# Kernel optimization log

Measured on AMD Instinct MI355X. Metric: run time of the kernel, lower is better.

## Reference

```python
import jax, jax.numpy as jnp
import numpy as np

N = 100000   # nodes
E = 1600000  # edges (avg degree 16)
Q = 64       # mesoscale velocity bins
H = 64       # collision MLP hidden dim
DT = 0.1
REG = 1e-6


def setup_inputs() -> dict:
    key = jax.random.key(0)
    ks = jax.random.split(key, 10)
    return {
        "f": jax.random.uniform(ks[0], (N, Q), jnp.float32),
        "macro_u": jax.random.normal(ks[1], (N, 1), jnp.float32),
        "source": 0.01 * jax.random.normal(ks[2], (N, Q), jnp.float32),
        "edge_src": jax.random.randint(ks[3], (E,), 0, N, jnp.int32),
        "edge_dst": jax.random.randint(ks[4], (E,), 0, N, jnp.int32),
        "edge_w": jax.random.uniform(ks[5], (E,), jnp.float32),
        "xi": jnp.linspace(-1.0, 1.0, Q).astype(jnp.float32),
        "w_in": jax.random.normal(ks[6], (Q, H), jnp.float32) / np.float32(np.sqrt(Q)),
        "b_in": jnp.zeros((H,), jnp.float32),
        "w_hid": jax.random.normal(ks[7], (3, H, H), jnp.float32) / np.float32(np.sqrt(H)),
        "b_hid": jnp.zeros((3, H), jnp.float32),
        "w_out": jax.random.normal(ks[8], (H, Q), jnp.float32) / np.float32(np.sqrt(H)),
        "b_out": jnp.zeros((Q,), jnp.float32),
    }


def _collision(f, macro_u, xi, w_in, b_in, w_hid, b_hid, w_out, b_out):
    # 5-layer MLP: relu hidden, tanh output (CollisionOperator.forward)
    x = jax.nn.relu(f @ w_in + b_in)
    for i in range(3):  # fixed small layer count, not a data-dim loop
        x = jax.nn.relu(x @ w_hid[i] + b_hid[i])
    omega = jnp.tanh(x @ w_out + b_out)                     # [N, Q]
    # Hard collision-invariance constraint: Omega* = (I - C^T (C C^T)^-1 C) Omega
    q = f.shape[1]
    w = jnp.full((q,), 1.0 / q, f.dtype)                    # quadrature weights
    xi_shifted = xi[None, :] + macro_u                      # [N, Q]
    C = jnp.stack([jnp.broadcast_to(w, xi_shifted.shape), w * xi_shifted], axis=1)  # [N,2,Q]
    CCT = jnp.einsum('naq,nbq->nab', C, C) + REG * jnp.eye(2, dtype=f.dtype)        # [N,2,2]
    v = jnp.einsum('naq,nq->na', C, omega)                  # [N,2]
    s = jnp.linalg.solve(CCT, v[..., None])[..., 0]         # [N,2]  (== CCT^-1 v)
    return omega - jnp.einsum('naq,na->nq', C, s)           # avoid dense [N,Q,Q] projection


def _transport(f, xi, edge_src, edge_dst, edge_w, n):
    # BoltzmannUpdater.compute_transport_term: both inflow (on graph) and
    # outflow (on reverse graph) reduce to the same per-edge message
    #   m_e = (w_e / out_deg[src_e]) * xi * (f[dst_e] - f[src_e])
    # aggregated at dst (inflow) and at src (outflow); transport = outflow - inflow.
    out_deg = jax.ops.segment_sum(jnp.ones_like(edge_w), edge_src, num_segments=n)
    q_e = edge_w / out_deg[edge_src]                         # [E]
    msg = q_e[:, None] * xi[None, :] * (f[edge_dst] - f[edge_src])  # [E, Q]
    inflow = jax.ops.segment_sum(msg, edge_dst, num_segments=n)
    outflow = jax.ops.segment_sum(msg, edge_src, num_segments=n)
    return outflow - inflow


def reference(f, macro_u, source, edge_src, edge_dst, edge_w, xi,
              w_in, b_in, w_hid, b_hid, w_out, b_out):
    f = jnp.maximum(f, 0.0)  # clamp(min=0)
    omega = _collision(f, macro_u, xi, w_in, b_in, w_hid, b_hid, w_out, b_out)
    trans = _transport(f, xi, edge_src, edge_dst, edge_w, f.shape[0])
    f_new = f - DT * (trans - omega - source)
    return jnp.maximum(f_new, 0.0)
```

## Files before the change

### kernel.cpp

```cpp
#include <hip/hip_runtime.h>

#define NN 100000
#define EE 1600000
#define DTc 0.1f
#define REGc 1e-6f
#define WQc (1.0f / 64.0f)

#define NB 782
#define CAP 4736
#define BS_NB 782
#define TENT (2 * EE)
#define ACT_S 72
#define PRE_NB 3125
#define WP_NB 80
#define SIDE_BIT (1u << 24)

typedef unsigned long long u64;
typedef __attribute__((ext_vector_type(8))) short short8;
typedef __attribute__((ext_vector_type(4))) float f32x4;

__device__ __forceinline__ unsigned short f2bf(float x) {
    unsigned u = __float_as_uint(x);
    unsigned r = (u + 0x7fffu + ((u >> 16) & 1u)) >> 16;
    return (unsigned short)r;
}
__device__ __forceinline__ float bf2f(unsigned short s) {
    return __uint_as_float(((unsigned)s) << 16);
}
__device__ __forceinline__ unsigned pack2(float a, float b) {
    return (unsigned)f2bf(fmaxf(a, 0.f)) | ((unsigned)f2bf(fmaxf(b, 0.f)) << 16);
}

__global__ __launch_bounds__(256) void prep_kernel(
    const float* __restrict__ f, unsigned int* __restrict__ fb16u,
    const float* __restrict__ w_in, const float* __restrict__ w_hid,
    const float* __restrict__ w_out, unsigned short* __restrict__ wp) {
    int b = blockIdx.x;
    if (b < PRE_NB) {
        int i = b * 256 + threadIdx.x;
        float4 v0 = *(const float4*)&f[i * 8];
        float4 v1 = *(const float4*)&f[i * 8 + 4];
        uint4 w;
        w.x = pack2(v0.x, v0.y);
        w.y = pack2(v0.z, v0.w);
        w.z = pack2(v1.x, v1.y);
        w.w = pack2(v1.z, v1.w);
        *(uint4*)&fb16u[i * 4] = w;
    } else {
        int i = (b - PRE_NB) * 256 + threadIdx.x;
        int l = i >> 12, idx = i & 4095;
        int n = idx >> 6, k = idx & 63;
        const float* W = (l == 0) ? w_in : (l < 4 ? w_hid + (l - 1) * 4096 : w_out);
        wp[i] = f2bf(W[k * 64 + n]);
    }
}

__global__ __launch_bounds__(256) void bin_scatter(
    const int* __restrict__ esrc, const int* __restrict__ edst,
    const float* __restrict__ ew, int* __restrict__ bcur,
    u64* __restrict__ adj64) {
    __shared__ int cnt[NB];
    __shared__ int bas[NB];
    int t = threadIdx.x, blk = blockIdx.x;
    for (int j = t; j < NB; j += 256) cnt[j] = 0;
    __syncthreads();
    int base = blk * 2048;
    int nE = min(2048, EE - base);
    int i = t * 8;
    bool act = (i < nE);
    int4 sa, sb, da, db;
    float4 wa, wb;
    if (act) {
        sa = *(const int4*)&esrc[base + i];
        sb = *(const int4*)&esrc[base + i + 4];
        da = *(const int4*)&edst[base + i];
        db = *(const int4*)&edst[base + i + 4];
        wa = *(const float4*)&ew[base + i];
        wb = *(const float4*)&ew[base + i + 4];
        atomicAdd(&cnt[sa.x >> 7], 1); atomicAdd(&cnt[da.x >> 7], 1);
        atomicAdd(&cnt[sa.y >> 7], 1); atomicAdd(&cnt[da.y >> 7], 1);
        atomicAdd(&cnt[sa.z >> 7], 1); atomicAdd(&cnt[da.z >> 7], 1);
        atomicAdd(&cnt[sa.w >> 7], 1); atomicAdd(&cnt[da.w >> 7], 1);
        atomicAdd(&cnt[sb.x >> 7], 1); atomicAdd(&cnt[db.x >> 7], 1);
        atomicAdd(&cnt[sb.y >> 7], 1); atomicAdd(&cnt[db.y >> 7], 1);
        atomicAdd(&cnt[sb.z >> 7], 1); atomicAdd(&cnt[db.z >> 7], 1);
        atomicAdd(&cnt[sb.w >> 7], 1); atomicAdd(&cnt[db.w >> 7], 1);
    }
    __syncthreads();
    for (int j = t; j < NB; j += 256) {
        int c = cnt[j];
        bas[j] = (c ? atomicAdd(&bcur[j], c) : 0) + j * CAP;
        cnt[j] = 0;
    }
    __syncthreads();
    if (act) {
#define EMIT(s, d, w)                                                         \
        {                                                                     \
            u64 wb64 = ((u64)__float_as_uint(w)) << 32;                       \
            int p1 = bas[(s) >> 7] + atomicAdd(&cnt[(s) >> 7], 1);            \
            adj64[p1] = wb64 | SIDE_BIT | (unsigned)((d) | (((s) & 127) << 17)); \
            int p2 = bas[(d) >> 7] + atomicAdd(&cnt[(d) >> 7], 1);            \
            adj64[p2] = wb64 | (unsigned)((s) | (((d) & 127) << 17));         \
        }
        EMIT(sa.x, da.x, wa.x) EMIT(sa.y, da.y, wa.y)
        EMIT(sa.z, da.z, wa.z) EMIT(sa.w, da.w, wa.w)
        EMIT(sb.x, db.x, wb.x) EMIT(sb.y, db.y, wb.y)
        EMIT(sb.z, db.z, wb.z) EMIT(sb.w, db.w, wb.w)
#undef EMIT
    }
}

__global__ __launch_bounds__(1024) void scan_nb(const int* __restrict__ bcur,
                                                int* __restrict__ cbase) {
    __shared__ int s[1024];
    int t = threadIdx.x;
    int v = (t < NB) ? bcur[t] : 0;
    s[t] = v;
    __syncthreads();
    for (int o = 1; o < 1024; o <<= 1) {
        int x = (t >= o) ? s[t - o] : 0;
        __syncthreads();
        s[t] += x;
        __syncthreads();
    }
    if (t < NB) cbase[t] = s[t] - v;
}

__global__ __launch_bounds__(256) void bucket_histo(
    const int* __restrict__ bcur, const int* __restrict__ cbase,
    const u64* __restrict__ adj64,
    int* __restrict__ node_offs, int* __restrict__ deg) {
    __shared__ int cnt_tot[128], cnt_src[128], sc[128];
    int t = threadIdx.x, b = blockIdx.x;
    if (t < 128) { cnt_tot[t] = 0; cnt_src[t] = 0; }
    __syncthreads();
    int used = bcur[b];
    int gstart = b * CAP;
    for (int i = t; i < used; i += 256) {
        unsigned lo = (unsigned)adj64[gstart + i];
        int local = (lo >> 17) & 127;
        atomicAdd(&cnt_tot[local], 1);
        if (lo & SIDE_BIT) atomicAdd(&cnt_src[local], 1);
    }
    __syncthreads();
    if (t < 128) sc[t] = cnt_tot[t];
    __syncthreads();
    for (int o = 1; o < 128; o <<= 1) {
        int x = 0;
        if (t < 128 && t >= o) x = sc[t - o];
        __syncthreads();
        if (t < 128) sc[t] += x;
        __syncthreads();
    }
    if (t < 128) {
        int n = b * 128 + t;
        if (n < NN) {
            node_offs[n] = cbase[b] + sc[t] - cnt_tot[t];
            deg[n] = cnt_src[t];
        }
    }
    if (b == 0 && t == 0) node_offs[NN] = TENT;
}

__global__ __launch_bounds__(256) void bucket_scatter(
    const int* __restrict__ bcur, const u64* __restrict__ adj64,
    const int* __restrict__ node_offs, const int* __restrict__ deg,
    unsigned int* __restrict__ adj4) {
    __shared__ int cur[128];
    __shared__ float ldeg[128];
    int t = threadIdx.x, b = blockIdx.x;
    if (t < 128) {
        int n = b * 128 + t;
        cur[t] = (n < NN) ? node_offs[n] : 0;
        ldeg[t] = (n < NN) ? (float)deg[n] : 1.f;
    }
    __syncthreads();
    int used = bcur[b];
    int gstart = b * CAP;
    for (int i = t; i < used; i += 256) {
        u64 e = adj64[gstart + i];
        unsigned lo = (unsigned)e;
        int local = (lo >> 17) & 127;
        unsigned other = lo & 0x1FFFFu;
        float w = __uint_as_float((unsigned)(e >> 32));
        float dv = (lo & SIDE_BIT) ? ldeg[local] : (float)deg[other];
        float q = w / dv;
        unsigned q15 = (unsigned)(q * 32768.f + 0.5f);
        if (q15 > 32767u) q15 = 32767u;
        int p = atomicAdd(&cur[local], 1);
        adj4[p] = (q15 << 17) | other;
    }
}

#define ACC8(q, r)                                          \
    a0 = fmaf(q, __uint_as_float(r.x << 16), a0);           \
    a1 = fmaf(q, __uint_as_float(r.x & 0xFFFF0000u), a1);   \
    a2 = fmaf(q, __uint_as_float(r.y << 16), a2);           \
    a3 = fmaf(q, __uint_as_float(r.y & 0xFFFF0000u), a3);   \
    a4 = fmaf(q, __uint_as_float(r.z << 16), a4);           \
    a5 = fmaf(q, __uint_as_float(r.z & 0xFFFF0000u), a5);   \
    a6 = fmaf(q, __uint_as_float(r.w << 16), a6);           \
    a7 = fmaf(q, __uint_as_float(r.w & 0xFFFF0000u), a7);   \
    qs += q;

__global__ __launch_bounds__(256) void gather_kernel(
    const unsigned int* __restrict__ fb16u, const int* __restrict__ node_offs,
    const unsigned int* __restrict__ adj, const float* __restrict__ xi,
    float* __restrict__ trans) {
    const float QS = 1.f / 32768.f;
    int lane = threadIdx.x & 63;
    int n = blockIdx.x * 4 + (threadIdx.x >> 6);
    if (n >= NN) return;
    int c = lane & 7;
    int qt = lane >> 3;
    int j = node_offs[n];
    int end = node_offs[n + 1];
    float a0 = 0.f, a1 = 0.f, a2 = 0.f, a3 = 0.f;
    float a4 = 0.f, a5 = 0.f, a6 = 0.f, a7 = 0.f, qs = 0.f;
    for (; j + 32 <= end; j += 32) {
        unsigned e0 = __builtin_nontemporal_load(&adj[j + qt]);
        unsigned e1 = __builtin_nontemporal_load(&adj[j + 8 + qt]);
        unsigned e2 = __builtin_nontemporal_load(&adj[j + 16 + qt]);
        unsigned e3 = __builtin_nontemporal_load(&adj[j + 24 + qt]);
        uint4 r0 = *(const uint4*)&fb16u[(e0 & 0x1FFFFu) * 32 + c * 4];
        uint4 r1 = *(const uint4*)&fb16u[(e1 & 0x1FFFFu) * 32 + c * 4];
        uint4 r2 = *(const uint4*)&fb16u[(e2 & 0x1FFFFu) * 32 + c * 4];
        uint4 r3 = *(const uint4*)&fb16u[(e3 & 0x1FFFFu) * 32 + c * 4];
        float q0 = (float)(e0 >> 17) * QS;
        float q1 = (float)(e1 >> 17) * QS;
        float q2 = (float)(e2 >> 17) * QS;
        float q3 = (float)(e3 >> 17) * QS;
        ACC8(q0, r0)
        ACC8(q1, r1)
        ACC8(q2, r2)
        ACC8(q3, r3)
    }
    for (; j + 8 <= end; j += 8) {
        unsigned e = __builtin_nontemporal_load(&adj[j + qt]);
        uint4 r = *(const uint4*)&fb16u[(e & 0x1FFFFu) * 32 + c * 4];
        float q = (float)(e >> 17) * QS;
        ACC8(q, r)
    }
    if (j < end) {
        int idx = j + qt;
        bool ok = idx < end;
        unsigned e = ok ? adj[idx] : 0u;
        uint4 r = *(const uint4*)&fb16u[(e & 0x1FFFFu) * 32 + c * 4];
        float q = ok ? (float)(e >> 17) * QS : 0.f;
        ACC8(q, r)
    }
#define RED3(x) x += __shfl_xor(x, 8); x += __shfl_xor(x, 16); x += __shfl_xor(x, 32)
    RED3(a0); RED3(a1); RED3(a2); RED3(a3);
    RED3(a4); RED3(a5); RED3(a6); RED3(a7); RED3(qs);
    if (qt == 0) {
        uint4 rn = *(const uint4*)&fb16u[n * 32 + c * 4];
        float4 x0 = *(const float4*)&xi[c * 8];
        float4 x1 = *(const float4*)&xi[c * 8 + 4];
        f32x4 o0, o1;
        o0.x = x0.x * (a0 - qs * __uint_as_float(rn.x << 16));
        o0.y = x0.y * (a1 - qs * __uint_as_float(rn.x & 0xFFFF0000u));
        o0.z = x0.z * (a2 - qs * __uint_as_float(rn.y << 16));
        o0.w = x0.w * (a3 - qs * __uint_as_float(rn.y & 0xFFFF0000u));
        o1.x = x1.x * (a4 - qs * __uint_as_float(rn.z << 16));
        o1.y = x1.y * (a5 - qs * __uint_as_float(rn.z & 0xFFFF0000u));
        o1.z = x1.z * (a6 - qs * __uint_as_float(rn.w << 16));
        o1.w = x1.w * (a7 - qs * __uint_as_float(rn.w & 0xFFFF0000u));
        __builtin_nontemporal_store(o0, (f32x4*)&trans[n * 64 + c * 8]);
        __builtin_nontemporal_store(o1, (f32x4*)&trans[n * 64 + c * 8 + 4]);
    }
}

__global__ __launch_bounds__(256) void node_kernel(
    const unsigned short* __restrict__ fb16, const float* __restrict__ f,
    const float* __restrict__ macro_u, const float* __restrict__ source,
    const float* __restrict__ xi, const unsigned short* __restrict__ wp,
    const float* __restrict__ b_in, const float* __restrict__ b_hid,
    const float* __restrict__ b_out,
    const float* __restrict__ trans, float* __restrict__ out) {
    __shared__ __attribute__((aligned(16))) unsigned short act[128 * ACT_S];
    __shared__ float s0s[128], s1s[128], us[128], xif[64];

    const int t = threadIdx.x;
    const int wid = t >> 6;
    const int lane = t & 63;
    const int m = lane & 15;
    const int quad = lane >> 4;
    const int nodeBase = blockIdx.x * 128;
    const int gbase = nodeBase * 64;

    if (t < 128) {
        int n = nodeBase + t;
        us[t] = (n < NN) ? macro_u[n] : 0.f;
    }
    if (t < 64) xif[t] = xi[t];

#pragma unroll
    for (int i = 0; i < 8; i++) {
        int r = wid * 32 + i * 4 + (lane >> 4);
        int c = (lane & 15) * 4;
        uint2 v = {0u, 0u};
        if (nodeBase + r < NN) v = *(const uint2*)&fb16[gbase + r * 64 + c];
        *(uint2*)&act[r * ACT_S + c] = v;
    }

    const int rowbase = wid * 32;

    for (int l = 0; l < 5; l++) {
        const unsigned short* W = wp + l * 4096;
        const float* B = (l == 0) ? b_in : (l < 4 ? b_hid + (l - 1) * 64 : b_out);

        short8 Af[2][2], Bf[4][2];
#pragma unroll
        for (int rt = 0; rt < 2; rt++)
#pragma unroll
            for (int kk = 0; kk < 2; kk++)
                Af[rt][kk] = *(const short8*)&act[(rowbase + rt * 16 + m) * ACT_S + kk * 32 + quad * 8];
#pragma unroll
        for (int ct = 0; ct < 4; ct++)
#pragma unroll
            for (int kk = 0; kk < 2; kk++)
                Bf[ct][kk] = *(const short8*)&W[(ct * 16 + m) * 64 + kk * 32 + quad * 8];

        f32x4 acc[2][4];
#pragma unroll
        for (int rt = 0; rt < 2; rt++)
#pragma unroll
            for (int ct = 0; ct < 4; ct++) {
                acc[rt][ct] = (f32x4){0.f, 0.f, 0.f, 0.f};
                acc[rt][ct] = __builtin_amdgcn_mfma_f32_16x16x32_bf16(Af[rt][0], Bf[ct][0], acc[rt][ct], 0, 0, 0);
                acc[rt][ct] = __builtin_amdgcn_mfma_f32_16x16x32_bf16(Af[rt][1], Bf[ct][1], acc[rt][ct], 0, 0, 0);
            }

#pragma unroll
        for (int rt = 0; rt < 2; rt++)
#pragma unroll
            for (int ct = 0; ct < 4; ct++) {
                float bv = B[ct * 16 + m];
#pragma unroll
                for (int r = 0; r < 4; r++) {
                    int row = rowbase + rt * 16 + quad * 4 + r;
                    float val = acc[rt][ct][r] + bv;
                    val = (l < 4) ? fmaxf(val, 0.f) : tanhf(val);
                    act[row * ACT_S + ct * 16 + m] = f2bf(val);
                }
            }
    }
    __syncthreads();

    if (t < 128) {
        float u = us[t];
        float v0 = 0.f, v1 = 0.f, sxs2 = 0.f, sxi = 0.f;
        const short8* rp = (const short8*)&act[t * ACT_S];
#pragma unroll
        for (int c = 0; c < 8; c++) {
            short8 v = rp[c];
#pragma unroll
            for (int jj = 0; jj < 8; jj++) {
                float om = bf2f((unsigned short)v[jj]);
                float xv = xif[c * 8 + jj];
                float xs = xv + u;
                v0 += om;
                v1 += xs * om;
                sxs2 += xs * xs;
                sxi += xv;
            }
        }
        v0 *= WQc;
        v1 *= WQc;
        float c00 = WQc + REGc;
        float c01 = WQc * WQc * (sxi + 64.f * u);
        float c11 = WQc * WQc * sxs2 + REGc;
        float det = c00 * c11 - c01 * c01;
        float inv = 1.0f / det;
        s0s[t] = (c11 * v0 - c01 * v1) * inv;
        s1s[t] = (c00 * v1 - c01 * v0) * inv;
    }
    __syncthreads();

#pragma unroll
    for (int i = 0; i < 8; i++) {
        int e = (i * 256 + t) * 4;
        int nl = e >> 6;
        if (nodeBase + nl < NN) {
            int g = gbase + e;
            int c0 = e & 63;
            float4 fv = *(const float4*)&f[g];
            float4 sv = *(const float4*)&source[g];
            float4 tv = *(const float4*)&trans[g];
            float uu = us[nl];
            float sv0 = s0s[nl], sv1 = s1s[nl];
            float4 ov;
            float* ovp = (float*)&ov;
            const float* fp = (const float*)&fv;
            const float* sp = (const float*)&sv;
            const float* tp = (const float*)&tv;
#pragma unroll
            for (int jj = 0; jj < 4; jj++) {
                float om = bf2f(act[nl * ACT_S + c0 + jj]);
                float xs = xif[c0 + jj] + uu;
                float omst = om - WQc * (sv0 + xs * sv1);
                float val = fmaxf(fp[jj], 0.f) + DTc * (sp[jj] + omst - tp[jj]);
                ovp[jj] = fmaxf(val, 0.f);
            }
            *(float4*)&out[g] = ov;
        }
    }
}

extern "C" void kernel_launch(void* const* d_in, const int* in_sizes, int n_in,
                              void* d_out, int out_size, void* d_ws, size_t ws_size,
                              hipStream_t stream) {
    const float* f       = (const float*)d_in[0];
    const float* macro_u = (const float*)d_in[1];
    const float* source  = (const float*)d_in[2];
    const int*   esrc    = (const int*)d_in[3];
    const int*   edst    = (const int*)d_in[4];
    const float* ew      = (const float*)d_in[5];
    const float* xi      = (const float*)d_in[6];
    const float* w_in    = (const float*)d_in[7];
    const float* b_in    = (const float*)d_in[8];
    const float* w_hid   = (const float*)d_in[9];
    const float* b_hid   = (const float*)d_in[10];
    const float* w_out   = (const float*)d_in[11];
    const float* b_out   = (const float*)d_in[12];
    float* out = (float*)d_out;

    u64* adj64 = (u64*)d_ws;
    unsigned int* adj4 = (unsigned int*)(adj64 + (size_t)NB * CAP);
    int* deg   = (int*)(adj4 + TENT);
    int* bcur  = deg + NN;
    int* cbase = bcur + 784;
    int* node_offs = cbase + 784;
    float* trans = (float*)(node_offs + NN + 8);
    unsigned short* fb16 = (unsigned short*)(trans + (size_t)NN * 64);
    unsigned short* wp = fb16 + (size_t)NN * 64;

    hipMemsetAsync(bcur, 0, 784 * sizeof(int), stream);

    prep_kernel<<<PRE_NB + WP_NB, 256, 0, stream>>>(
        f, (unsigned int*)fb16, w_in, w_hid, w_out, wp);
    bin_scatter<<<BS_NB, 256, 0, stream>>>(esrc, edst, ew, bcur, adj64);
    scan_nb<<<1, 1024, 0, stream>>>(bcur, cbase);
    bucket_histo<<<NB, 256, 0, stream>>>(bcur, cbase, adj64, node_offs, deg);
    bucket_scatter<<<NB, 256, 0, stream>>>(bcur, adj64, node_offs, deg, adj4);
    gather_kernel<<<(NN + 3) / 4, 256, 0, stream>>>((const unsigned int*)fb16,
                                                    node_offs, adj4, xi, trans);
    node_kernel<<<(NN + 127) / 128, 256, 0, stream>>>(
        fb16, f, macro_u, source, xi, wp, b_in, b_hid, b_out, trans, out);
}
```

Measured before the change: 336.8 us.

## Fuse edge binning into prep kernel and drop global bucket scan

Moves the edge bin-scatter into prep_kernel as extra blocks so binning and the bf16 conversion of f run in one launch. Removes the scan_nb kernel by leaving the compacted CSR with gaps: each bucket keeps its fixed CAP-sized region, and per-node start and end offsets are stored separately. This saves two kernel launches and a serialization point, at the cost of a sparser adj4 array (NB*CAP entries) and an extra end-offset read per node in the gather.

Measured after the change: 331.6 us. About the same (-1.5%).

```diff
diff --git a/kernel.cpp b/kernel.cpp
--- a/kernel.cpp
+++ b/kernel.cpp
@@ -9,7 +9,6 @@
 #define NB 782
 #define CAP 4736
 #define BS_NB 782
-#define TENT (2 * EE)
 #define ACT_S 72
 #define PRE_NB 3125
 #define WP_NB 80
@@ -34,10 +33,63 @@
 __global__ __launch_bounds__(256) void prep_kernel(
     const float* __restrict__ f, unsigned int* __restrict__ fb16u,
     const float* __restrict__ w_in, const float* __restrict__ w_hid,
-    const float* __restrict__ w_out, unsigned short* __restrict__ wp) {
+    const float* __restrict__ w_out, unsigned short* __restrict__ wp,
+    const int* __restrict__ esrc, const int* __restrict__ edst,
+    const float* __restrict__ ew, int* __restrict__ bcur,
+    u64* __restrict__ adj64) {
     int b = blockIdx.x;
-    if (b < PRE_NB) {
-        int i = b * 256 + threadIdx.x;
+    if (b < BS_NB) {
+        __shared__ int cnt[NB];
+        __shared__ int bas[NB];
+        int t = threadIdx.x;
+        for (int j = t; j < NB; j += 256) cnt[j] = 0;
+        __syncthreads();
+        int base = b * 2048;
+        int nE = min(2048, EE - base);
+        int i = t * 8;
+        bool act = (i < nE);
+        int4 sa, sb, da, db;
+        float4 wa, wb;
+        if (act) {
+            sa = *(const int4*)&esrc[base + i];
+            sb = *(const int4*)&esrc[base + i + 4];
+            da = *(const int4*)&edst[base + i];
+            db = *(const int4*)&edst[base + i + 4];
+            wa = *(const float4*)&ew[base + i];
+            wb = *(const float4*)&ew[base + i + 4];
+            atomicAdd(&cnt[sa.x >> 7], 1); atomicAdd(&cnt[da.x >> 7], 1);
+            atomicAdd(&cnt[sa.y >> 7], 1); atomicAdd(&cnt[da.y >> 7], 1);
+            atomicAdd(&cnt[sa.z >> 7], 1); atomicAdd(&cnt[da.z >> 7], 1);
+            atomicAdd(&cnt[sa.w >> 7], 1); atomicAdd(&cnt[da.w >> 7], 1);
+            atomicAdd(&cnt[sb.x >> 7], 1); atomicAdd(&cnt[db.x >> 7], 1);
+            atomicAdd(&cnt[sb.y >> 7], 1); atomicAdd(&cnt[db.y >> 7], 1);
+            atomicAdd(&cnt[sb.z >> 7], 1); atomicAdd(&cnt[db.z >> 7], 1);
+            atomicAdd(&cnt[sb.w >> 7], 1); atomicAdd(&cnt[db.w >> 7], 1);
+        }
+        __syncthreads();
+        for (int j = t; j < NB; j += 256) {
+            int c = cnt[j];
+            bas[j] = (c ? atomicAdd(&bcur[j], c) : 0) + j * CAP;
+            cnt[j] = 0;
+        }
+        __syncthreads();
+        if (act) {
+#define EMIT(s, d, w)                                                         \
+            {                                                                 \
+                u64 wb64 = ((u64)__float_as_uint(w)) << 32;                   \
+                int p1 = bas[(s) >> 7] + atomicAdd(&cnt[(s) >> 7], 1);        \
+                adj64[p1] = wb64 | SIDE_BIT | (unsigned)((d) | (((s) & 127) << 17)); \
+                int p2 = bas[(d) >> 7] + atomicAdd(&cnt[(d) >> 7], 1);        \
+                adj64[p2] = wb64 | (unsigned)((s) | (((d) & 127) << 17));     \
+            }
+            EMIT(sa.x, da.x, wa.x) EMIT(sa.y, da.y, wa.y)
+            EMIT(sa.z, da.z, wa.z) EMIT(sa.w, da.w, wa.w)
+            EMIT(sb.x, db.x, wb.x) EMIT(sb.y, db.y, wb.y)
+            EMIT(sb.z, db.z, wb.z) EMIT(sb.w, db.w, wb.w)
+#undef EMIT
+        }
+    } else if (b < BS_NB + PRE_NB) {
+        int i = (b - BS_NB) * 256 + threadIdx.x;
         float4 v0 = *(const float4*)&f[i * 8];
         float4 v1 = *(const float4*)&f[i * 8 + 4];
         uint4 w;
@@ -47,7 +99,7 @@
         w.w = pack2(v1.z, v1.w);
         *(uint4*)&fb16u[i * 4] = w;
     } else {
-        int i = (b - PRE_NB) * 256 + threadIdx.x;
+        int i = (b - BS_NB - PRE_NB) * 256 + threadIdx.x;
         int l = i >> 12, idx = i & 4095;
         int n = idx >> 6, k = idx & 63;
         const float* W = (l == 0) ? w_in : (l < 4 ? w_hid + (l - 1) * 4096 : w_out);
@@ -55,81 +107,10 @@
     }
 }
 
-__global__ __launch_bounds__(256) void bin_scatter(
-    const int* __restrict__ esrc, const int* __restrict__ edst,
-    const float* __restrict__ ew, int* __restrict__ bcur,
-    u64* __restrict__ adj64) {
-    __shared__ int cnt[NB];
-    __shared__ int bas[NB];
-    int t = threadIdx.x, blk = blockIdx.x;
-    for (int j = t; j < NB; j += 256) cnt[j] = 0;
-    __syncthreads();
-    int base = blk * 2048;
-    int nE = min(2048, EE - base);
-    int i = t * 8;
-    bool act = (i < nE);
-    int4 sa, sb, da, db;
-    float4 wa, wb;
-    if (act) {
-        sa = *(const int4*)&esrc[base + i];
-        sb = *(const int4*)&esrc[base + i + 4];
-        da = *(const int4*)&edst[base + i];
-        db = *(const int4*)&edst[base + i + 4];
-        wa = *(const float4*)&ew[base + i];
-        wb = *(const float4*)&ew[base + i + 4];
-        atomicAdd(&cnt[sa.x >> 7], 1); atomicAdd(&cnt[da.x >> 7], 1);
-        atomicAdd(&cnt[sa.y >> 7], 1); atomicAdd(&cnt[da.y >> 7], 1);
-        atomicAdd(&cnt[sa.z >> 7], 1); atomicAdd(&cnt[da.z >> 7], 1);
-        atomicAdd(&cnt[sa.w >> 7], 1); atomicAdd(&cnt[da.w >> 7], 1);
-        atomicAdd(&cnt[sb.x >> 7], 1); atomicAdd(&cnt[db.x >> 7], 1);
-        atomicAdd(&cnt[sb.y >> 7], 1); atomicAdd(&cnt[db.y >> 7], 1);
-        atomicAdd(&cnt[sb.z >> 7], 1); atomicAdd(&cnt[db.z >> 7], 1);
-        atomicAdd(&cnt[sb.w >> 7], 1); atomicAdd(&cnt[db.w >> 7], 1);
-    }
-    __syncthreads();
-    for (int j = t; j < NB; j += 256) {
-        int c = cnt[j];
-        bas[j] = (c ? atomicAdd(&bcur[j], c) : 0) + j * CAP;
-        cnt[j] = 0;
-    }
-    __syncthreads();
-    if (act) {
-#define EMIT(s, d, w)                                                         \
-        {                                                                     \
-            u64 wb64 = ((u64)__float_as_uint(w)) << 32;                       \
-            int p1 = bas[(s) >> 7] + atomicAdd(&cnt[(s) >> 7], 1);            \
-            adj64[p1] = wb64 | SIDE_BIT | (unsigned)((d) | (((s) & 127) << 17)); \
-            int p2 = bas[(d) >> 7] + atomicAdd(&cnt[(d) >> 7], 1);            \
-            adj64[p2] = wb64 | (unsigned)((s) | (((d) & 127) << 17));         \
-        }
-        EMIT(sa.x, da.x, wa.x) EMIT(sa.y, da.y, wa.y)
-        EMIT(sa.z, da.z, wa.z) EMIT(sa.w, da.w, wa.w)
-        EMIT(sb.x, db.x, wb.x) EMIT(sb.y, db.y, wb.y)
-        EMIT(sb.z, db.z, wb.z) EMIT(sb.w, db.w, wb.w)
-#undef EMIT
-    }
-}
-
-__global__ __launch_bounds__(1024) void scan_nb(const int* __restrict__ bcur,
-                                                int* __restrict__ cbase) {
-    __shared__ int s[1024];
-    int t = threadIdx.x;
-    int v = (t < NB) ? bcur[t] : 0;
-    s[t] = v;
-    __syncthreads();
-    for (int o = 1; o < 1024; o <<= 1) {
-        int x = (t >= o) ? s[t - o] : 0;
-        __syncthreads();
-        s[t] += x;
-        __syncthreads();
-    }
-    if (t < NB) cbase[t] = s[t] - v;
-}
-
 __global__ __launch_bounds__(256) void bucket_histo(
-    const int* __restrict__ bcur, const int* __restrict__ cbase,
-    const u64* __restrict__ adj64,
-    int* __restrict__ node_offs, int* __restrict__ deg) {
+    const int* __restrict__ bcur, const u64* __restrict__ adj64,
+    int* __restrict__ node_offs, int* __restrict__ node_end,
+    int* __restrict__ deg) {
     __shared__ int cnt_tot[128], cnt_src[128], sc[128];
     int t = threadIdx.x, b = blockIdx.x;
     if (t < 128) { cnt_tot[t] = 0; cnt_src[t] = 0; }
@@ -155,11 +136,11 @@
     if (t < 128) {
         int n = b * 128 + t;
         if (n < NN) {
-            node_offs[n] = cbase[b] + sc[t] - cnt_tot[t];
+            node_offs[n] = gstart + sc[t] - cnt_tot[t];
+            node_end[n]  = gstart + sc[t];
             deg[n] = cnt_src[t];
         }
     }
-    if (b == 0 && t == 0) node_offs[NN] = TENT;
 }
 
 __global__ __launch_bounds__(256) void bucket_scatter(
@@ -205,6 +186,7 @@
 
 __global__ __launch_bounds__(256) void gather_kernel(
     const unsigned int* __restrict__ fb16u, const int* __restrict__ node_offs,
+    const int* __restrict__ node_end,
     const unsigned int* __restrict__ adj, const float* __restrict__ xi,
     float* __restrict__ trans) {
     const float QS = 1.f / 32768.f;
@@ -214,7 +196,7 @@
     int c = lane & 7;
     int qt = lane >> 3;
     int j = node_offs[n];
-    int end = node_offs[n + 1];
+    int end = node_end[n];
     float a0 = 0.f, a1 = 0.f, a2 = 0.f, a3 = 0.f;
     float a4 = 0.f, a5 = 0.f, a6 = 0.f, a7 = 0.f, qs = 0.f;
     for (; j + 32 <= end; j += 32) {
@@ -427,24 +409,22 @@
 
     u64* adj64 = (u64*)d_ws;
     unsigned int* adj4 = (unsigned int*)(adj64 + (size_t)NB * CAP);
-    int* deg   = (int*)(adj4 + TENT);
-    int* bcur  = deg + NN;
-    int* cbase = bcur + 784;
-    int* node_offs = cbase + 784;
-    float* trans = (float*)(node_offs + NN + 8);
+    int* deg   = (int*)(adj4 + (size_t)NB * CAP);
+    int* node_offs = deg + NN;
+    int* node_end  = node_offs + NN;
+    int* bcur  = node_end + NN;
+    float* trans = (float*)(bcur + 784);
     unsigned short* fb16 = (unsigned short*)(trans + (size_t)NN * 64);
     unsigned short* wp = fb16 + (size_t)NN * 64;
 
     hipMemsetAsync(bcur, 0, 784 * sizeof(int), stream);
 
-    prep_kernel<<<PRE_NB + WP_NB, 256, 0, stream>>>(
-        f, (unsigned int*)fb16, w_in, w_hid, w_out, wp);
-    bin_scatter<<<BS_NB, 256, 0, stream>>>(esrc, edst, ew, bcur, adj64);
-    scan_nb<<<1, 1024, 0, stream>>>(bcur, cbase);
-    bucket_histo<<<NB, 256, 0, stream>>>(bcur, cbase, adj64, node_offs, deg);
+    prep_kernel<<<BS_NB + PRE_NB + WP_NB, 256, 0, stream>>>(
+        f, (unsigned int*)fb16, w_in, w_hid, w_out, wp, esrc, edst, ew, bcur, adj64);
+    bucket_histo<<<NB, 256, 0, stream>>>(bcur, adj64, node_offs, node_end, deg);
     bucket_scatter<<<NB, 256, 0, stream>>>(bcur, adj64, node_offs, deg, adj4);
     gather_kernel<<<(NN + 3) / 4, 256, 0, stream>>>((const unsigned int*)fb16,
-                                                    node_offs, adj4, xi, trans);
+                                                    node_offs, node_end, adj4, xi, trans);
     node_kernel<<<(NN + 127) / 128, 256, 0, stream>>>(
         fb16, f, macro_u, source, xi, wp, b_in, b_hid, b_out, trans, out);
 }
```
